# Optimization experiments

Measured on AMD Instinct MI355X. Metric: run time of the kernel, lower is better.

## Reference

```python
import jax, jax.numpy as jnp
import numpy as np

NP_, NA_, NS_ = 4096, 4096, 1
E_ = 131072
DIN, DOUT, H = 256, 64, 4
SLOPE = 0.2  # leaky relu negative slope


def _leaky(x):
    return jnp.where(x >= 0, x, SLOPE * x)


def setup_inputs() -> dict:
    key = jax.random.key(0)
    ks = iter(jax.random.split(key, 64))
    inp = {}
    inp['feat_P'] = jax.random.normal(next(ks), (NP_, DIN), jnp.float32)
    inp['feat_A'] = jax.random.normal(next(ks), (NA_, DIN), jnp.float32)
    inp['feat_state'] = jax.random.normal(next(ks), (NS_, DIN), jnp.float32)
    for name in ['P', 'A', 'p2p', 'p2a', 'a2p', 'a2a', 'p2s', 'a2s', 'in']:
        inp['W_' + name] = jax.random.normal(next(ks), (DOUT * H, DIN), jnp.float32) / np.sqrt(DIN)
        inp['b_' + name] = jax.random.normal(next(ks), (DOUT * H,), jnp.float32) * 0.01
    for name in ['p2p', 'p2a', 'a2p', 'a2a', 'p2s', 'a2s']:
        inp['att_%s_src' % name] = jax.random.normal(next(ks), (1, H, DOUT), jnp.float32) * 0.1
        inp['att_%s_dst' % name] = jax.random.normal(next(ks), (1, H, DOUT), jnp.float32) * 0.1
    for name, ns, nd in [('p2p', NP_, NP_), ('p2a', NP_, NA_), ('a2p', NA_, NP_), ('a2a', NA_, NA_)]:
        inp['e_%s_src' % name] = jax.random.randint(next(ks), (E_,), 0, ns, jnp.int32)
        inp['e_%s_dst' % name] = jax.random.randint(next(ks), (E_,), 0, nd, jnp.int32)
    inp['e_p2s_src'] = jnp.arange(NP_, dtype=jnp.int32)
    inp['e_p2s_dst'] = jnp.zeros((NP_,), jnp.int32)
    inp['e_a2s_src'] = jnp.arange(NA_, dtype=jnp.int32)
    inp['e_a2s_dst'] = jnp.zeros((NA_,), jnp.int32)
    return inp


def _msg_agg(feat_src, W, b, att_s, att_d, Wh_dst, src, dst, n_dst):
    # per-edge lossy_u_mul_e with comm_loss == 0 (noise branch dead):
    # gather src features, per-edge linear, per-edge softmax over HEADS (torch Softmax(dim=1)).
    h = feat_src[src]                                    # [E, DIN]
    Wh = (h @ W.T + b).reshape(-1, H, DOUT)              # [E, H, D]
    a_s = jnp.sum(Wh * att_s, axis=-1, keepdims=True)    # [E, H, 1]
    a_d = jnp.sum(Wh_dst[dst] * att_d, axis=-1, keepdims=True)
    attn = jax.nn.softmax(_leaky(a_s + a_d), axis=1)     # softmax over heads, as in original
    return jax.ops.segment_sum(Wh * attn, dst, num_segments=n_dst)


def _edge_softmax_agg(Wh_src, att_s, Wh_state, att_d, src, dst, n_dst):
    # dgl edge_softmax: destination-grouped stable softmax over incoming edges.
    a_s = jnp.sum(Wh_src * att_s, axis=-1, keepdims=True)[src]    # [E, H, 1]
    a_d = jnp.sum(Wh_state * att_d, axis=-1, keepdims=True)[dst]  # [E, H, 1]
    e = _leaky(a_s + a_d)
    m = jax.ops.segment_max(e, dst, num_segments=n_dst)
    ex = jnp.exp(e - m[dst])
    den = jax.ops.segment_sum(ex, dst, num_segments=n_dst)
    a = ex / den[dst]
    return jax.ops.segment_sum(Wh_src[src] * a, dst, num_segments=n_dst)


def reference(feat_P, feat_A, feat_state,
              W_P, b_P, W_A, b_A, W_p2p, b_p2p, W_p2a, b_p2a, W_a2p, b_a2p,
              W_a2a, b_a2a, W_p2s, b_p2s, W_a2s, b_a2s, W_in, b_in,
              att_p2p_src, att_p2p_dst, att_p2a_src, att_p2a_dst,
              att_a2p_src, att_a2p_dst, att_a2a_src, att_a2a_dst,
              att_p2s_src, att_p2s_dst, att_a2s_src, att_a2s_dst,
              e_p2p_src, e_p2p_dst, e_p2a_src, e_p2a_dst,
              e_a2p_src, e_a2p_dst, e_a2a_src, e_a2a_dst,
              e_p2s_src, e_p2s_dst, e_a2s_src, e_a2s_dst):
    Whp = (feat_P @ W_P.T + b_P).reshape(NP_, H, DOUT)
    Wha = (feat_A @ W_A.T + b_A).reshape(NA_, H, DOUT)
    Whp2s = (feat_P @ W_p2s.T + b_p2s).reshape(NP_, H, DOUT)
    Wha2s = (feat_A @ W_a2s.T + b_a2s).reshape(NA_, H, DOUT)
    Whin = (feat_state @ W_in.T + b_in).reshape(NS_, H, DOUT)

    ft_p2p = _msg_agg(feat_P, W_p2p, b_p2p, att_p2p_src, att_p2p_dst, Whp, e_p2p_src, e_p2p_dst, NP_)
    ft_p2a = _msg_agg(feat_P, W_p2a, b_p2a, att_p2a_src, att_p2a_dst, Wha, e_p2a_src, e_p2a_dst, NA_)
    ft_a2p = _msg_agg(feat_A, W_a2p, b_a2p, att_a2p_src, att_a2p_dst, Whp, e_a2p_src, e_a2p_dst, NP_)
    ft_a2a = _msg_agg(feat_A, W_a2a, b_a2a, att_a2a_src, att_a2a_dst, Wha, e_a2a_src, e_a2a_dst, NA_)

    ft_p2s = _edge_softmax_agg(Whp2s, att_p2s_src, Whin, att_p2s_dst, e_p2s_src, e_p2s_dst, NS_)
    ft_a2s = _edge_softmax_agg(Wha2s, att_a2s_src, Whin, att_a2s_dst, e_a2s_src, e_a2s_dst, NS_)

    h_P = jax.nn.relu(Whp + ft_p2p + ft_a2p)
    h_A = jax.nn.relu(Wha + ft_p2a + ft_a2a)
    h_S = jax.nn.relu(Whin + ft_p2s + ft_a2s)
    return (h_P, h_A, h_S)
```

## Files before the change

kernel.cpp:

```cpp
#include <hip/hip_runtime.h>

#define NPA   4096
#define DHD   256
#define EDG   131072
#define OS    4104
#define TBL_SZ ((size_t)NPA * DHD)

#define B_AH    ((size_t)0)
#define B_WH    (B_AH + 2 * TBL_SZ * 2)
#define B_TBL   (B_WH + (size_t)8 * 65536 * 2)
#define B_SCORE (B_TBL + 8 * TBL_SZ * 2)
#define B_CNT   (B_SCORE + (size_t)10 * NPA * 4 * 4)
#define B_OFFS  (B_CNT + (size_t)4 * NPA * 4)
#define B_CUR   (B_OFFS + (size_t)4 * OS * 4)
#define B_PKT   (B_CUR + (size_t)4 * NPA * 4)
#define B_WHIN  (B_PKT + (size_t)4 * EDG * 16)
#define B_SCD   (B_WHIN + 256 * 4)
#define B_DEN   (B_SCD + 8 * 4)
#define B_NUM   (B_DEN + 8 * 4)

typedef _Float16 half8 __attribute__((ext_vector_type(8)));
typedef _Float16 half4 __attribute__((ext_vector_type(4)));
typedef _Float16 half2v __attribute__((ext_vector_type(2)));
typedef float floatx4 __attribute__((ext_vector_type(4)));

struct CastArgs { const float* src[10]; };
struct GemmArgs {
    const float* b[8];
    const float* att0[8]; const float* att1[8];
    int sj0[8]; int sj1[8];
};
struct EdgeArgs { const int* src[4]; const int* dst[4]; };

__device__ __forceinline__ float lrelu(float x) { return x >= 0.0f ? x : 0.2f * x; }

__device__ __forceinline__ int pack2(float a, float b) {
    half2v h = {(_Float16)a, (_Float16)b};
    return __builtin_bit_cast(int, h);
}
__device__ __forceinline__ half2v bc2(int v) { return __builtin_bit_cast(half2v, v); }

__device__ __forceinline__ half2v asplat(const int4& p, int head) {
    int w = (head & 2) ? p.z : p.y;
    int b = (head & 1) ? ((w >> 16) & 0xffff) : (w & 0xffff);
    return bc2(b | (b << 16));
}

__global__ __launch_bounds__(256) void cast_kernel(CastArgs ca, _Float16* __restrict__ dst) {
    size_t i4 = ((size_t)blockIdx.x * 256 + threadIdx.x) * 4;
    const float* s; size_t off;
    if (i4 < TBL_SZ)            { s = ca.src[0]; off = i4; }
    else if (i4 < 2 * TBL_SZ)   { s = ca.src[1]; off = i4 - TBL_SZ; }
    else { size_t r = i4 - 2 * TBL_SZ; s = ca.src[2 + (r >> 16)]; off = r & 65535; }
    float4 v = *(const float4*)(s + off);
    half4 h = {(_Float16)v.x, (_Float16)v.y, (_Float16)v.z, (_Float16)v.w};
    *(half4*)(dst + i4) = h;
}

__global__ __launch_bounds__(256) void aux_kernel(EdgeArgs ea,
        const float* __restrict__ fs, const float* __restrict__ Win,
        const float* __restrict__ bin, const float* __restrict__ attP,
        const float* __restrict__ attA,
        int* __restrict__ cnt, float* __restrict__ whin, float* __restrict__ scd) {
    int bid = blockIdx.x;
    int wave = threadIdx.x >> 6, lane = threadIdx.x & 63;
    if (bid < 64) {
        int o = bid * 4 + wave;
        float4 w = *(const float4*)&Win[(size_t)o * 256 + lane * 4];
        float4 f = *(const float4*)&fs[lane * 4];
        float v = w.x * f.x + w.y * f.y + w.z * f.z + w.w * f.w;
        for (int d = 32; d; d >>= 1) v += __shfl_xor(v, d);
        if (lane == 0) {
            v += bin[o];
            whin[o] = v;
            atomicAdd(&scd[o >> 6], v * attP[o]);
            atomicAdd(&scd[4 + (o >> 6)], v * attA[o]);
        }
        return;
    }
    int tid = (bid - 64) * 256 + threadIdx.x;
    for (int idx = tid; idx < 4 * EDG; idx += 192 * 256) {
        int r = idx >> 17;
        int e = idx & (EDG - 1);
        atomicAdd(&cnt[r * NPA + ea.dst[r][e]], 1);
    }
}

__global__ __launch_bounds__(256) void gemm_kernel(const _Float16* __restrict__ Ah,
        const _Float16* __restrict__ Whb, GemmArgs ga,
        _Float16* __restrict__ tblBase, float* __restrict__ score) {
    int j = blockIdx.x >> 6;
    int mt = blockIdx.x & 63;
    int w = threadIdx.x >> 6, lane = threadIdx.x & 63;
    int quad = lane >> 4, l16 = lane & 15;
    const _Float16* A = Ah + (size_t)(j >> 2) * TBL_SZ;
    const _Float16* W = Whb + (size_t)j * 65536;
    const float* bias = ga.b[j];
    _Float16* out = tblBase + (size_t)j * TBL_SZ;
    int mr0 = mt * 64;
    int nc0 = w * 64;
    const _Float16* ap[4];
    const _Float16* bp[4];
#pragma unroll
    for (int g = 0; g < 4; ++g) {
        ap[g] = A + (size_t)(mr0 + g * 16 + l16) * 256 + quad * 8;
        bp[g] = W + (size_t)(nc0 + g * 16 + l16) * 256 + quad * 8;
    }
    floatx4 acc[4][4];
#pragma unroll
    for (int rg = 0; rg < 4; ++rg)
#pragma unroll
        for (int cg = 0; cg < 4; ++cg) acc[rg][cg] = (floatx4){0, 0, 0, 0};
#pragma unroll
    for (int k0 = 0; k0 < 256; k0 += 32) {
        half8 av[4], bv[4];
#pragma unroll
        for (int g = 0; g < 4; ++g) av[g] = *(const half8*)(ap[g] + k0);
#pragma unroll
        for (int g = 0; g < 4; ++g) bv[g] = *(const half8*)(bp[g] + k0);
#pragma unroll
        for (int rg = 0; rg < 4; ++rg)
#pragma unroll
            for (int cg = 0; cg < 4; ++cg)
                acc[rg][cg] = __builtin_amdgcn_mfma_f32_16x16x32_f16(av[rg], bv[cg], acc[rg][cg], 0, 0, 0);
    }
    float bc[4];
#pragma unroll
    for (int cg = 0; cg < 4; ++cg) bc[cg] = bias[nc0 + cg * 16 + l16];
#pragma unroll
    for (int rg = 0; rg < 4; ++rg)
#pragma unroll
        for (int i = 0; i < 4; ++i) {
            int row = mr0 + rg * 16 + quad * 4 + i;
#pragma unroll
            for (int cg = 0; cg < 4; ++cg)
                out[(size_t)row * 256 + nc0 + cg * 16 + l16] = (_Float16)(acc[rg][cg][i] + bc[cg]);
        }
#pragma unroll
    for (int tt = 0; tt < 2; ++tt) {
        const float* att = tt ? ga.att1[j] : ga.att0[j];
        int sj = tt ? ga.sj1[j] : ga.sj0[j];
        if (!att) continue;
        float at[4];
#pragma unroll
        for (int cg = 0; cg < 4; ++cg) at[cg] = att[nc0 + cg * 16 + l16];
        float* sb = score + (size_t)sj * NPA * 4;
#pragma unroll
        for (int rg = 0; rg < 4; ++rg)
#pragma unroll
            for (int i = 0; i < 4; ++i) {
                float p = (acc[rg][0][i] + bc[0]) * at[0] + (acc[rg][1][i] + bc[1]) * at[1]
                        + (acc[rg][2][i] + bc[2]) * at[2] + (acc[rg][3][i] + bc[3]) * at[3];
                p += __shfl_xor(p, 1); p += __shfl_xor(p, 2);
                p += __shfl_xor(p, 4); p += __shfl_xor(p, 8);
                if (l16 == 0) {
                    int row = mr0 + rg * 16 + quad * 4 + i;
                    sb[(size_t)row * 4 + w] = p;
                }
            }
    }
}

__global__ __launch_bounds__(1024) void scan_kernel(const int* __restrict__ counts,
                                                    int* __restrict__ offs, int* __restrict__ cur) {
    int r = blockIdx.x;
    int t = threadIdx.x;
    int wave = t >> 6, lane = t & 63;
    int4 v = *(const int4*)&counts[(size_t)r * NPA + t * 4];
    int lsum = v.x + v.y + v.z + v.w;
    int s = lsum;
#pragma unroll
    for (int d = 1; d < 64; d <<= 1) {
        int u = __shfl_up(s, d);
        if (lane >= d) s += u;
    }
    __shared__ int wsum[16];
    if (lane == 63) wsum[wave] = s;
    __syncthreads();
    if (wave == 0 && lane < 16) {
        int wv = wsum[lane];
#pragma unroll
        for (int d = 1; d < 16; d <<= 1) {
            int u = __shfl_up(wv, d);
            if (lane >= d) wv += u;
        }
        wsum[lane] = wv;
    }
    __syncthreads();
    int base = (wave ? wsum[wave - 1] : 0) + s - lsum;
    int4 ov = {base, base + v.x, base + v.x + v.y, base + v.x + v.y + v.z};
    *(int4*)&offs[(size_t)r * OS + t * 4] = ov;
    *(int4*)&cur[(size_t)r * NPA + t * 4] = ov;
    if (t == 1023) offs[(size_t)r * OS + NPA] = base + lsum;
}

__global__ __launch_bounds__(256) void scatter_attn(EdgeArgs ea, const float* __restrict__ scoreBase,
        int* __restrict__ cur, int4* __restrict__ pkt) {
    int idx = (blockIdx.x * 256 + threadIdx.x) * 2;
    int r = idx >> 17;
    int e = idx & (EDG - 1);
    int2 s2 = *(const int2*)&ea.src[r][e];
    int2 d2 = *(const int2*)&ea.dst[r][e];
    const float* as = scoreBase + (size_t)r * NPA * 4;
    const float* ad = scoreBase + (size_t)(4 + r) * NPA * 4;
    float4 av0 = *(const float4*)&as[(size_t)s2.x * 4];
    float4 dv0 = *(const float4*)&ad[(size_t)d2.x * 4];
    float4 av1 = *(const float4*)&as[(size_t)s2.y * 4];
    float4 dv1 = *(const float4*)&ad[(size_t)d2.y * 4];
#pragma unroll
    for (int u = 0; u < 2; ++u) {
        float4 av = u ? av1 : av0;
        float4 dv = u ? dv1 : dv0;
        int s = u ? s2.y : s2.x;
        int d = u ? d2.y : d2.x;
        float x0 = lrelu(av.x + dv.x), x1 = lrelu(av.y + dv.y);
        float x2 = lrelu(av.z + dv.z), x3 = lrelu(av.w + dv.w);
        float m = fmaxf(fmaxf(x0, x1), fmaxf(x2, x3));
        float e0 = __expf(x0 - m), e1 = __expf(x1 - m), e2 = __expf(x2 - m), e3 = __expf(x3 - m);
        float inv = 1.0f / (e0 + e1 + e2 + e3);
        int pos = atomicAdd(&cur[r * NPA + d], 1);
        int4 pk = {s, pack2(e0 * inv, e1 * inv), pack2(e2 * inv, e3 * inv), 0};
        pkt[(size_t)r * EDG + pos] = pk;
    }
}

__global__ __launch_bounds__(256) void agg_kernel(const int* __restrict__ offs,
        const int4* __restrict__ pkt, const _Float16* __restrict__ tblBase,
        float* __restrict__ outBase) {
    int side = blockIdx.y;
    int wave = threadIdx.x >> 6, lane = threadIdx.x & 63;
    int dn = blockIdx.x * 4 + wave;
    int h = lane >> 5, l32 = lane & 31;
    int head = l32 >> 3;
    half2v accA[4] = {{0,0},{0,0},{0,0},{0,0}};
    half2v accB[4] = {{0,0},{0,0},{0,0},{0,0}};
    const int srcIdx[4] = {1, 2, 5, 6};
    const int4 z = {0, 0, 0, 0};
#pragma unroll
    for (int q = 0; q < 2; ++q) {
        int r = side + q * 2;
        const int* of = offs + (size_t)r * OS;
        const int4* pkb = pkt + (size_t)r * EDG;
        const _Float16* wh = tblBase + (size_t)srcIdx[r] * TBL_SZ;
        int beg = of[dn], end = of[dn + 1];
        int i = beg;
        int4 p0 = (i + h     < end) ? pkb[i + h]     : z;
        int4 p1 = (i + 2 + h < end) ? pkb[i + 2 + h] : z;
        int4 p2 = (i + 4 + h < end) ? pkb[i + 4 + h] : z;
        int4 p3 = (i + 6 + h < end) ? pkb[i + 6 + h] : z;
        while (i < end) {
            int ni = i + 8;
            half8 w0 = *(const half8*)(wh + (size_t)p0.x * 256 + l32 * 8);
            half8 w1 = *(const half8*)(wh + (size_t)p1.x * 256 + l32 * 8);
            half8 w2 = *(const half8*)(wh + (size_t)p2.x * 256 + l32 * 8);
            half8 w3 = *(const half8*)(wh + (size_t)p3.x * 256 + l32 * 8);
            int4 n0 = (ni + h     < end) ? pkb[ni + h]     : z;
            int4 n1 = (ni + 2 + h < end) ? pkb[ni + 2 + h] : z;
            int4 n2 = (ni + 4 + h < end) ? pkb[ni + 4 + h] : z;
            int4 n3 = (ni + 6 + h < end) ? pkb[ni + 6 + h] : z;
            half2v a0 = asplat(p0, head), a1 = asplat(p1, head);
            half2v a2 = asplat(p2, head), a3 = asplat(p3, head);
            int4 i0 = __builtin_bit_cast(int4, w0);
            int4 i1 = __builtin_bit_cast(int4, w1);
            int4 i2 = __builtin_bit_cast(int4, w2);
            int4 i3 = __builtin_bit_cast(int4, w3);
            accA[0] += bc2(i0.x) * a0; accA[1] += bc2(i0.y) * a0;
            accA[2] += bc2(i0.z) * a0; accA[3] += bc2(i0.w) * a0;
            accB[0] += bc2(i1.x) * a1; accB[1] += bc2(i1.y) * a1;
            accB[2] += bc2(i1.z) * a1; accB[3] += bc2(i1.w) * a1;
            accA[0] += bc2(i2.x) * a2; accA[1] += bc2(i2.y) * a2;
            accA[2] += bc2(i2.z) * a2; accA[3] += bc2(i2.w) * a2;
            accB[0] += bc2(i3.x) * a3; accB[1] += bc2(i3.y) * a3;
            accB[2] += bc2(i3.z) * a3; accB[3] += bc2(i3.w) * a3;
            p0 = n0; p1 = n1; p2 = n2; p3 = n3;
            i = ni;
        }
    }
    float f[8];
#pragma unroll
    for (int k = 0; k < 4; ++k) {
        half2v s = accA[k] + accB[k];
        f[2 * k] = (float)s[0];
        f[2 * k + 1] = (float)s[1];
    }
#pragma unroll
    for (int k = 0; k < 8; ++k) f[k] += __shfl_xor(f[k], 32);
    if (h == 0) {
        const _Float16* skip = tblBase + (size_t)(side * 4) * TBL_SZ + (size_t)dn * 256 + l32 * 8;
        half8 sv = *(const half8*)skip;
        float* op = outBase + ((size_t)side * NPA + dn) * 256 + l32 * 8;
        float4 o0 = {fmaxf(f[0] + (float)sv[0], 0.f), fmaxf(f[1] + (float)sv[1], 0.f),
                     fmaxf(f[2] + (float)sv[2], 0.f), fmaxf(f[3] + (float)sv[3], 0.f)};
        float4 o1 = {fmaxf(f[4] + (float)sv[4], 0.f), fmaxf(f[5] + (float)sv[5], 0.f),
                     fmaxf(f[6] + (float)sv[6], 0.f), fmaxf(f[7] + (float)sv[7], 0.f)};
        *(float4*)op = o0;
        *(float4*)(op + 4) = o1;
    }
}

__global__ __launch_bounds__(256) void state_kernel(const _Float16* __restrict__ tblBase,
        const float* __restrict__ scoreBase, const float* __restrict__ scd,
        float* __restrict__ den, float* __restrict__ num) {
    int r = blockIdx.y;
    int blk = blockIdx.x;
    int t = threadIdx.x;
    int h = t >> 6;
    const _Float16* wh = tblBase + (size_t)(r == 0 ? 3 : 7) * TBL_SZ;
    const float* as = scoreBase + (size_t)(8 + r) * NPA * 4;
    float dh = scd[r * 4 + h];
    float dsum = 0.0f, acc = 0.0f;
    for (int i = blk; i < NPA; i += 128) {
        float x = lrelu(as[(size_t)i * 4 + h] + dh);
        float w = __expf(x);
        dsum += w;
        acc += w * (float)wh[(size_t)i * 256 + t];
    }
    atomicAdd(&num[r * 256 + t], acc);
    if ((t & 63) == 0) atomicAdd(&den[r * 4 + h], dsum);
}

__global__ __launch_bounds__(256) void state_final(const float* __restrict__ whin,
        const float* __restrict__ den, const float* __restrict__ num, float* __restrict__ out) {
    int t = threadIdx.x;
    int h = t >> 6;
    float v = whin[t] + num[t] / den[h] + num[256 + t] / den[4 + h];
    out[t] = v > 0.0f ? v : 0.0f;
}

extern "C" void kernel_launch(void* const* d_in, const int* in_sizes, int n_in,
                              void* d_out, int out_size, void* d_ws, size_t ws_size,
                              hipStream_t stream) {
    auto F = [&](int i) { return (const float*)d_in[i]; };
    char* ws = (char*)d_ws;
    _Float16* Ah  = (_Float16*)(ws + B_AH);
    _Float16* Whb = (_Float16*)(ws + B_WH);
    _Float16* tbl = (_Float16*)(ws + B_TBL);
    float* score  = (float*)(ws + B_SCORE);
    int* cnt      = (int*)(ws + B_CNT);
    int* offs     = (int*)(ws + B_OFFS);
    int* cur      = (int*)(ws + B_CUR);
    int4* pkt     = (int4*)(ws + B_PKT);
    float* whin   = (float*)(ws + B_WHIN);
    float* scd    = (float*)(ws + B_SCD);
    float* den    = (float*)(ws + B_DEN);
    float* num    = (float*)(ws + B_NUM);

    (void)hipMemsetAsync(cnt, 0, (size_t)4 * NPA * 4, stream);
    (void)hipMemsetAsync(scd, 0, (8 + 8 + 512) * sizeof(float), stream);

    CastArgs ca = {{F(0), F(1), F(3), F(7), F(9), F(15), F(5), F(11), F(13), F(17)}};
    cast_kernel<<<2560, 256, 0, stream>>>(ca, Ah);

    GemmArgs ga;
    const int bIdx[8] = {4, 8, 10, 16, 6, 12, 14, 18};
    for (int j = 0; j < 8; ++j) ga.b[j] = F(bIdx[j]);
    const int a0Idx[8]  = {22, 21, 23, 29, 24, 25, 27, 31};
    const int sj0Arr[8] = { 4,  0,  1,  8,  5,  2,  3,  9};
    for (int j = 0; j < 8; ++j) {
        ga.att0[j] = F(a0Idx[j]); ga.sj0[j] = sj0Arr[j];
        ga.att1[j] = nullptr;     ga.sj1[j] = -1;
    }
    ga.att1[0] = F(26); ga.sj1[0] = 6;
    ga.att1[4] = F(28); ga.sj1[4] = 7;

    EdgeArgs ea = {{(const int*)d_in[33], (const int*)d_in[35], (const int*)d_in[37], (const int*)d_in[39]},
                   {(const int*)d_in[34], (const int*)d_in[36], (const int*)d_in[38], (const int*)d_in[40]}};

    aux_kernel<<<256, 256, 0, stream>>>(ea, F(2), F(19), F(20), F(30), F(32), cnt, whin, scd);
    gemm_kernel<<<512, 256, 0, stream>>>(Ah, Whb, ga, tbl, score);

    scan_kernel<<<4, 1024, 0, stream>>>(cnt, offs, cur);
    scatter_attn<<<1024, 256, 0, stream>>>(ea, score, cur, pkt);
    agg_kernel<<<dim3(1024, 2), 256, 0, stream>>>(offs, pkt, tbl, (float*)d_out);
    state_kernel<<<dim3(128, 2), 256, 0, stream>>>(tbl, score, scd, den, num);
    state_final<<<1, 256, 0, stream>>>(whin, den, num, (float*)d_out + 2 * TBL_SZ);
}
```

Baseline: 278.4 us.

## Move edge attention into aggregation, fuse cast/aux kernels and state finalize

The scatter pass now writes only a 4-byte source-index permutation instead of 16-byte packets carrying precomputed attention. The aggregation kernel gathers source scores itself and computes the per-head softmax there, and the destination scores are loaded once per node. The cast and aux kernels become one launch, state_final is folded into state_kernel through a last-block ticket, and the two memsets become one. This cuts launches and scatter write traffic, but adds redundant exp work and extra score gathers inside the aggregation loop. Softmax also drops max-subtraction, which could overflow on large scores.

Result: slower. 309.0 us (+11.0%).

```diff
diff --git a/kernel.cpp b/kernel.cpp
--- a/kernel.cpp
+++ b/kernel.cpp
@@ -11,13 +11,15 @@
 #define B_TBL   (B_WH + (size_t)8 * 65536 * 2)
 #define B_SCORE (B_TBL + 8 * TBL_SZ * 2)
 #define B_CNT   (B_SCORE + (size_t)10 * NPA * 4 * 4)
-#define B_OFFS  (B_CNT + (size_t)4 * NPA * 4)
-#define B_CUR   (B_OFFS + (size_t)4 * OS * 4)
-#define B_PKT   (B_CUR + (size_t)4 * NPA * 4)
-#define B_WHIN  (B_PKT + (size_t)4 * EDG * 16)
-#define B_SCD   (B_WHIN + 256 * 4)
+#define B_SCD   (B_CNT + (size_t)4 * NPA * 4)
 #define B_DEN   (B_SCD + 8 * 4)
 #define B_NUM   (B_DEN + 8 * 4)
+#define B_TKT   (B_NUM + 512 * 4)
+#define B_ZEND  (B_TKT + 16)
+#define B_OFFS  (B_ZEND)
+#define B_CUR   (B_OFFS + (size_t)4 * OS * 4)
+#define B_PERM  (B_CUR + (size_t)4 * NPA * 4)
+#define B_WHIN  (B_PERM + (size_t)4 * EDG * 4)
 
 typedef _Float16 half8 __attribute__((ext_vector_type(8)));
 typedef _Float16 half4 __attribute__((ext_vector_type(4)));
@@ -33,39 +35,40 @@
 struct EdgeArgs { const int* src[4]; const int* dst[4]; };
 
 __device__ __forceinline__ float lrelu(float x) { return x >= 0.0f ? x : 0.2f * x; }
-
-__device__ __forceinline__ int pack2(float a, float b) {
-    half2v h = {(_Float16)a, (_Float16)b};
-    return __builtin_bit_cast(int, h);
-}
 __device__ __forceinline__ half2v bc2(int v) { return __builtin_bit_cast(half2v, v); }
-
-__device__ __forceinline__ half2v asplat(const int4& p, int head) {
-    int w = (head & 2) ? p.z : p.y;
-    int b = (head & 1) ? ((w >> 16) & 0xffff) : (w & 0xffff);
-    return bc2(b | (b << 16));
-}
-
-__global__ __launch_bounds__(256) void cast_kernel(CastArgs ca, _Float16* __restrict__ dst) {
-    size_t i4 = ((size_t)blockIdx.x * 256 + threadIdx.x) * 4;
-    const float* s; size_t off;
-    if (i4 < TBL_SZ)            { s = ca.src[0]; off = i4; }
-    else if (i4 < 2 * TBL_SZ)   { s = ca.src[1]; off = i4 - TBL_SZ; }
-    else { size_t r = i4 - 2 * TBL_SZ; s = ca.src[2 + (r >> 16)]; off = r & 65535; }
-    float4 v = *(const float4*)(s + off);
-    half4 h = {(_Float16)v.x, (_Float16)v.y, (_Float16)v.z, (_Float16)v.w};
-    *(half4*)(dst + i4) = h;
-}
-
-__global__ __launch_bounds__(256) void aux_kernel(EdgeArgs ea,
+__device__ __forceinline__ half2v cvt2(float a, float b) {
+    return __builtin_bit_cast(half2v, __builtin_amdgcn_cvt_pkrtz(a, b));
+}
+
+__device__ __forceinline__ float attn_head(float4 g, float4 ad, int head) {
+    float e0 = __expf(lrelu(g.x + ad.x));
+    float e1 = __expf(lrelu(g.y + ad.y));
+    float e2 = __expf(lrelu(g.z + ad.z));
+    float e3 = __expf(lrelu(g.w + ad.w));
+    float sel = (head & 2) ? ((head & 1) ? e3 : e2) : ((head & 1) ? e1 : e0);
+    return sel * __builtin_amdgcn_rcpf(e0 + e1 + e2 + e3);
+}
+
+__global__ __launch_bounds__(256) void prep_kernel(CastArgs ca, EdgeArgs ea,
         const float* __restrict__ fs, const float* __restrict__ Win,
         const float* __restrict__ bin, const float* __restrict__ attP,
-        const float* __restrict__ attA,
+        const float* __restrict__ attA, _Float16* __restrict__ dst,
         int* __restrict__ cnt, float* __restrict__ whin, float* __restrict__ scd) {
     int bid = blockIdx.x;
+    if (bid < 2560) {
+        size_t i4 = ((size_t)bid * 256 + threadIdx.x) * 4;
+        const float* s; size_t off;
+        if (i4 < TBL_SZ)            { s = ca.src[0]; off = i4; }
+        else if (i4 < 2 * TBL_SZ)   { s = ca.src[1]; off = i4 - TBL_SZ; }
+        else { size_t r = i4 - 2 * TBL_SZ; s = ca.src[2 + (r >> 16)]; off = r & 65535; }
+        float4 v = *(const float4*)(s + off);
+        half4 hh = {(_Float16)v.x, (_Float16)v.y, (_Float16)v.z, (_Float16)v.w};
+        *(half4*)(dst + i4) = hh;
+        return;
+    }
     int wave = threadIdx.x >> 6, lane = threadIdx.x & 63;
-    if (bid < 64) {
-        int o = bid * 4 + wave;
+    if (bid < 2624) {
+        int o = (bid - 2560) * 4 + wave;
         float4 w = *(const float4*)&Win[(size_t)o * 256 + lane * 4];
         float4 f = *(const float4*)&fs[lane * 4];
         float v = w.x * f.x + w.y * f.y + w.z * f.z + w.w * f.w;
@@ -78,7 +81,7 @@
         }
         return;
     }
-    int tid = (bid - 64) * 256 + threadIdx.x;
+    int tid = (bid - 2624) * 256 + threadIdx.x;
     for (int idx = tid; idx < 4 * EDG; idx += 192 * 256) {
         int r = idx >> 17;
         int e = idx & (EDG - 1);
@@ -194,39 +197,22 @@
     if (t == 1023) offs[(size_t)r * OS + NPA] = base + lsum;
 }
 
-__global__ __launch_bounds__(256) void scatter_attn(EdgeArgs ea, const float* __restrict__ scoreBase,
-        int* __restrict__ cur, int4* __restrict__ pkt) {
+__global__ __launch_bounds__(256) void scatter_kernel(EdgeArgs ea, int* __restrict__ cur,
+                                                      int* __restrict__ perm) {
     int idx = (blockIdx.x * 256 + threadIdx.x) * 2;
     int r = idx >> 17;
     int e = idx & (EDG - 1);
     int2 s2 = *(const int2*)&ea.src[r][e];
     int2 d2 = *(const int2*)&ea.dst[r][e];
-    const float* as = scoreBase + (size_t)r * NPA * 4;
-    const float* ad = scoreBase + (size_t)(4 + r) * NPA * 4;
-    float4 av0 = *(const float4*)&as[(size_t)s2.x * 4];
-    float4 dv0 = *(const float4*)&ad[(size_t)d2.x * 4];
-    float4 av1 = *(const float4*)&as[(size_t)s2.y * 4];
-    float4 dv1 = *(const float4*)&ad[(size_t)d2.y * 4];
-#pragma unroll
-    for (int u = 0; u < 2; ++u) {
-        float4 av = u ? av1 : av0;
-        float4 dv = u ? dv1 : dv0;
-        int s = u ? s2.y : s2.x;
-        int d = u ? d2.y : d2.x;
-        float x0 = lrelu(av.x + dv.x), x1 = lrelu(av.y + dv.y);
-        float x2 = lrelu(av.z + dv.z), x3 = lrelu(av.w + dv.w);
-        float m = fmaxf(fmaxf(x0, x1), fmaxf(x2, x3));
-        float e0 = __expf(x0 - m), e1 = __expf(x1 - m), e2 = __expf(x2 - m), e3 = __expf(x3 - m);
-        float inv = 1.0f / (e0 + e1 + e2 + e3);
-        int pos = atomicAdd(&cur[r * NPA + d], 1);
-        int4 pk = {s, pack2(e0 * inv, e1 * inv), pack2(e2 * inv, e3 * inv), 0};
-        pkt[(size_t)r * EDG + pos] = pk;
-    }
+    int p0 = atomicAdd(&cur[r * NPA + d2.x], 1);
+    perm[(size_t)r * EDG + p0] = s2.x;
+    int p1 = atomicAdd(&cur[r * NPA + d2.y], 1);
+    perm[(size_t)r * EDG + p1] = s2.y;
 }
 
 __global__ __launch_bounds__(256) void agg_kernel(const int* __restrict__ offs,
-        const int4* __restrict__ pkt, const _Float16* __restrict__ tblBase,
-        float* __restrict__ outBase) {
+        const int* __restrict__ perm, const float* __restrict__ score,
+        const _Float16* __restrict__ tblBase, float* __restrict__ outBase) {
     int side = blockIdx.y;
     int wave = threadIdx.x >> 6, lane = threadIdx.x & 63;
     int dn = blockIdx.x * 4 + wave;
@@ -235,44 +221,53 @@
     half2v accA[4] = {{0,0},{0,0},{0,0},{0,0}};
     half2v accB[4] = {{0,0},{0,0},{0,0},{0,0}};
     const int srcIdx[4] = {1, 2, 5, 6};
-    const int4 z = {0, 0, 0, 0};
 #pragma unroll
     for (int q = 0; q < 2; ++q) {
         int r = side + q * 2;
         const int* of = offs + (size_t)r * OS;
-        const int4* pkb = pkt + (size_t)r * EDG;
+        const int* pm = perm + (size_t)r * EDG;
+        const float* ss = score + (size_t)r * NPA * 4;
+        float4 ad = *(const float4*)&score[(size_t)(4 + r) * NPA * 4 + (size_t)dn * 4];
         const _Float16* wh = tblBase + (size_t)srcIdx[r] * TBL_SZ;
         int beg = of[dn], end = of[dn + 1];
         int i = beg;
-        int4 p0 = (i + h     < end) ? pkb[i + h]     : z;
-        int4 p1 = (i + 2 + h < end) ? pkb[i + 2 + h] : z;
-        int4 p2 = (i + 4 + h < end) ? pkb[i + 4 + h] : z;
-        int4 p3 = (i + 6 + h < end) ? pkb[i + 6 + h] : z;
+        int s0 = (i + h     < end) ? pm[i + h]     : 0;
+        int s1 = (i + 2 + h < end) ? pm[i + 2 + h] : 0;
+        int s2 = (i + 4 + h < end) ? pm[i + 4 + h] : 0;
+        int s3 = (i + 6 + h < end) ? pm[i + 6 + h] : 0;
         while (i < end) {
             int ni = i + 8;
-            half8 w0 = *(const half8*)(wh + (size_t)p0.x * 256 + l32 * 8);
-            half8 w1 = *(const half8*)(wh + (size_t)p1.x * 256 + l32 * 8);
-            half8 w2 = *(const half8*)(wh + (size_t)p2.x * 256 + l32 * 8);
-            half8 w3 = *(const half8*)(wh + (size_t)p3.x * 256 + l32 * 8);
-            int4 n0 = (ni + h     < end) ? pkb[ni + h]     : z;
-            int4 n1 = (ni + 2 + h < end) ? pkb[ni + 2 + h] : z;
-            int4 n2 = (ni + 4 + h < end) ? pkb[ni + 4 + h] : z;
-            int4 n3 = (ni + 6 + h < end) ? pkb[ni + 6 + h] : z;
-            half2v a0 = asplat(p0, head), a1 = asplat(p1, head);
-            half2v a2 = asplat(p2, head), a3 = asplat(p3, head);
+            float4 g0 = *(const float4*)&ss[(size_t)s0 * 4];
+            float4 g1 = *(const float4*)&ss[(size_t)s1 * 4];
+            float4 g2 = *(const float4*)&ss[(size_t)s2 * 4];
+            float4 g3 = *(const float4*)&ss[(size_t)s3 * 4];
+            half8 w0 = *(const half8*)(wh + (size_t)s0 * 256 + l32 * 8);
+            half8 w1 = *(const half8*)(wh + (size_t)s1 * 256 + l32 * 8);
+            half8 w2 = *(const half8*)(wh + (size_t)s2 * 256 + l32 * 8);
+            half8 w3 = *(const half8*)(wh + (size_t)s3 * 256 + l32 * 8);
+            int t0 = (ni + h     < end) ? pm[ni + h]     : 0;
+            int t1 = (ni + 2 + h < end) ? pm[ni + 2 + h] : 0;
+            int t2 = (ni + 4 + h < end) ? pm[ni + 4 + h] : 0;
+            int t3 = (ni + 6 + h < end) ? pm[ni + 6 + h] : 0;
+            float a0 = (i + h     < end) ? attn_head(g0, ad, head) : 0.f;
+            float a1 = (i + 2 + h < end) ? attn_head(g1, ad, head) : 0.f;
+            float a2 = (i + 4 + h < end) ? attn_head(g2, ad, head) : 0.f;
+            float a3 = (i + 6 + h < end) ? attn_head(g3, ad, head) : 0.f;
+            half2v ha0 = cvt2(a0, a0), ha1 = cvt2(a1, a1);
+            half2v ha2 = cvt2(a2, a2), ha3 = cvt2(a3, a3);
             int4 i0 = __builtin_bit_cast(int4, w0);
             int4 i1 = __builtin_bit_cast(int4, w1);
             int4 i2 = __builtin_bit_cast(int4, w2);
             int4 i3 = __builtin_bit_cast(int4, w3);
-            accA[0] += bc2(i0.x) * a0; accA[1] += bc2(i0.y) * a0;
-            accA[2] += bc2(i0.z) * a0; accA[3] += bc2(i0.w) * a0;
-            accB[0] += bc2(i1.x) * a1; accB[1] += bc2(i1.y) * a1;
-            accB[2] += bc2(i1.z) * a1; accB[3] += bc2(i1.w) * a1;
-            accA[0] += bc2(i2.x) * a2; accA[1] += bc2(i2.y) * a2;
-            accA[2] += bc2(i2.z) * a2; accA[3] += bc2(i2.w) * a2;
-            accB[0] += bc2(i3.x) * a3; accB[1] += bc2(i3.y) * a3;
-            accB[2] += bc2(i3.z) * a3; accB[3] += bc2(i3.w) * a3;
-            p0 = n0; p1 = n1; p2 = n2; p3 = n3;
+            accA[0] += bc2(i0.x) * ha0; accA[1] += bc2(i0.y) * ha0;
+            accA[2] += bc2(i0.z) * ha0; accA[3] += bc2(i0.w) * ha0;
+            accB[0] += bc2(i1.x) * ha1; accB[1] += bc2(i1.y) * ha1;
+            accB[2] += bc2(i1.z) * ha1; accB[3] += bc2(i1.w) * ha1;
+            accA[0] += bc2(i2.x) * ha2; accA[1] += bc2(i2.y) * ha2;
+            accA[2] += bc2(i2.z) * ha2; accA[3] += bc2(i2.w) * ha2;
+            accB[0] += bc2(i3.x) * ha3; accB[1] += bc2(i3.y) * ha3;
+            accB[2] += bc2(i3.z) * ha3; accB[3] += bc2(i3.w) * ha3;
+            s0 = t0; s1 = t1; s2 = t2; s3 = t3;
             i = ni;
         }
     }
@@ -299,14 +294,15 @@
 }
 
 __global__ __launch_bounds__(256) void state_kernel(const _Float16* __restrict__ tblBase,
-        const float* __restrict__ scoreBase, const float* __restrict__ scd,
-        float* __restrict__ den, float* __restrict__ num) {
+        const float* __restrict__ score, const float* __restrict__ scd,
+        float* __restrict__ den, float* __restrict__ num,
+        const float* __restrict__ whin, float* __restrict__ out, int* __restrict__ ticket) {
     int r = blockIdx.y;
     int blk = blockIdx.x;
     int t = threadIdx.x;
     int h = t >> 6;
     const _Float16* wh = tblBase + (size_t)(r == 0 ? 3 : 7) * TBL_SZ;
-    const float* as = scoreBase + (size_t)(8 + r) * NPA * 4;
+    const float* as = score + (size_t)(8 + r) * NPA * 4;
     float dh = scd[r * 4 + h];
     float dsum = 0.0f, acc = 0.0f;
     for (int i = blk; i < NPA; i += 128) {
@@ -317,14 +313,18 @@
     }
     atomicAdd(&num[r * 256 + t], acc);
     if ((t & 63) == 0) atomicAdd(&den[r * 4 + h], dsum);
-}
-
-__global__ __launch_bounds__(256) void state_final(const float* __restrict__ whin,
-        const float* __restrict__ den, const float* __restrict__ num, float* __restrict__ out) {
-    int t = threadIdx.x;
-    int h = t >> 6;
-    float v = whin[t] + num[t] / den[h] + num[256 + t] / den[4 + h];
-    out[t] = v > 0.0f ? v : 0.0f;
+    __threadfence();
+    __shared__ int last;
+    if (t == 0) last = (atomicAdd(ticket, 1) == 255);
+    __syncthreads();
+    if (last) {
+        float n0 = atomicAdd(&num[t], 0.f);
+        float n1 = atomicAdd(&num[256 + t], 0.f);
+        float d0 = atomicAdd(&den[h], 0.f);
+        float d1 = atomicAdd(&den[4 + h], 0.f);
+        float v = whin[t] + n0 / d0 + n1 / d1;
+        out[t] = fmaxf(v, 0.f);
+    }
 }
 
 extern "C" void kernel_launch(void* const* d_in, const int* in_sizes, int n_in,
@@ -337,19 +337,23 @@
     _Float16* tbl = (_Float16*)(ws + B_TBL);
     float* score  = (float*)(ws + B_SCORE);
     int* cnt      = (int*)(ws + B_CNT);
-    int* offs     = (int*)(ws + B_OFFS);
-    int* cur      = (int*)(ws + B_CUR);
-    int4* pkt     = (int4*)(ws + B_PKT);
-    float* whin   = (float*)(ws + B_WHIN);
     float* scd    = (float*)(ws + B_SCD);
     float* den    = (float*)(ws + B_DEN);
     float* num    = (float*)(ws + B_NUM);
-
-    (void)hipMemsetAsync(cnt, 0, (size_t)4 * NPA * 4, stream);
-    (void)hipMemsetAsync(scd, 0, (8 + 8 + 512) * sizeof(float), stream);
+    int* ticket   = (int*)(ws + B_TKT);
+    int* offs     = (int*)(ws + B_OFFS);
+    int* cur      = (int*)(ws + B_CUR);
+    int* perm     = (int*)(ws + B_PERM);
+    float* whin   = (float*)(ws + B_WHIN);
+
+    (void)hipMemsetAsync(ws + B_CNT, 0, B_ZEND - B_CNT, stream);
 
     CastArgs ca = {{F(0), F(1), F(3), F(7), F(9), F(15), F(5), F(11), F(13), F(17)}};
-    cast_kernel<<<2560, 256, 0, stream>>>(ca, Ah);
+    EdgeArgs ea = {{(const int*)d_in[33], (const int*)d_in[35], (const int*)d_in[37], (const int*)d_in[39]},
+                   {(const int*)d_in[34], (const int*)d_in[36], (const int*)d_in[38], (const int*)d_in[40]}};
+
+    prep_kernel<<<2816, 256, 0, stream>>>(ca, ea, F(2), F(19), F(20), F(30), F(32),
+                                          Ah, cnt, whin, scd);
 
     GemmArgs ga;
     const int bIdx[8] = {4, 8, 10, 16, 6, 12, 14, 18};
@@ -363,15 +367,10 @@
     ga.att1[0] = F(26); ga.sj1[0] = 6;
     ga.att1[4] = F(28); ga.sj1[4] = 7;
 
-    EdgeArgs ea = {{(const int*)d_in[33], (const int*)d_in[35], (const int*)d_in[37], (const int*)d_in[39]},
-                   {(const int*)d_in[34], (const int*)d_in[36], (const int*)d_in[38], (const int*)d_in[40]}};
-
-    aux_kernel<<<256, 256, 0, stream>>>(ea, F(2), F(19), F(20), F(30), F(32), cnt, whin, scd);
     gemm_kernel<<<512, 256, 0, stream>>>(Ah, Whb, ga, tbl, score);
-
     scan_kernel<<<4, 1024, 0, stream>>>(cnt, offs, cur);
-    scatter_attn<<<1024, 256, 0, stream>>>(ea, score, cur, pkt);
-    agg_kernel<<<dim3(1024, 2), 256, 0, stream>>>(offs, pkt, tbl, (float*)d_out);
-    state_kernel<<<dim3(128, 2), 256, 0, stream>>>(tbl, score, scd, den, num);
-    state_final<<<1, 256, 0, stream>>>(whin, den, num, (float*)d_out + 2 * TBL_SZ);
-}
+    scatter_kernel<<<1024, 256, 0, stream>>>(ea, cur, perm);
+    agg_kernel<<<dim3(1024, 2), 256, 0, stream>>>(offs, perm, score, tbl, (float*)d_out);
+    state_kernel<<<dim3(128, 2), 256, 0, stream>>>(tbl, score, scd, den, num, whin,
+                                                   (float*)d_out + 2 * TBL_SZ, ticket);
+}
```

## Fuse cast and aux kernels, use LDS histogram, merge memsets

Applied to the files above, without the earlier changes.

Merges the fp16 cast kernel and the aux kernel (state projection plus in-degree counting) into one prep kernel. This removes one launch, and the two memsets become a single memset by making the zeroed buffers contiguous. Degree counting now builds a per-block shared-memory histogram over 16K-edge chunks and flushes nonzero bins with global atomics. This replaces per-edge global atomics and cuts atomic contention, at the cost of 16KB of LDS per block and only 32 blocks doing the counting.

Measured after the change: 269.6 us. -3.1%, faster.

```diff
diff --git a/kernel.cpp b/kernel.cpp
--- a/kernel.cpp
+++ b/kernel.cpp
@@ -11,13 +11,14 @@
 #define B_TBL   (B_WH + (size_t)8 * 65536 * 2)
 #define B_SCORE (B_TBL + 8 * TBL_SZ * 2)
 #define B_CNT   (B_SCORE + (size_t)10 * NPA * 4 * 4)
-#define B_OFFS  (B_CNT + (size_t)4 * NPA * 4)
+#define B_SCD   (B_CNT + (size_t)4 * NPA * 4)
+#define B_DEN   (B_SCD + 8 * 4)
+#define B_NUM   (B_DEN + 8 * 4)
+#define B_ZEND  (B_NUM + 512 * 4)
+#define B_OFFS  (B_ZEND)
 #define B_CUR   (B_OFFS + (size_t)4 * OS * 4)
 #define B_PKT   (B_CUR + (size_t)4 * NPA * 4)
 #define B_WHIN  (B_PKT + (size_t)4 * EDG * 16)
-#define B_SCD   (B_WHIN + 256 * 4)
-#define B_DEN   (B_SCD + 8 * 4)
-#define B_NUM   (B_DEN + 8 * 4)
 
 typedef _Float16 half8 __attribute__((ext_vector_type(8)));
 typedef _Float16 half4 __attribute__((ext_vector_type(4)));
@@ -46,26 +47,36 @@
     return bc2(b | (b << 16));
 }
 
-__global__ __launch_bounds__(256) void cast_kernel(CastArgs ca, _Float16* __restrict__ dst) {
-    size_t i4 = ((size_t)blockIdx.x * 256 + threadIdx.x) * 4;
-    const float* s; size_t off;
-    if (i4 < TBL_SZ)            { s = ca.src[0]; off = i4; }
-    else if (i4 < 2 * TBL_SZ)   { s = ca.src[1]; off = i4 - TBL_SZ; }
-    else { size_t r = i4 - 2 * TBL_SZ; s = ca.src[2 + (r >> 16)]; off = r & 65535; }
-    float4 v = *(const float4*)(s + off);
-    half4 h = {(_Float16)v.x, (_Float16)v.y, (_Float16)v.z, (_Float16)v.w};
-    *(half4*)(dst + i4) = h;
-}
-
-__global__ __launch_bounds__(256) void aux_kernel(EdgeArgs ea,
+__global__ __launch_bounds__(256) void prep_kernel(CastArgs ca, EdgeArgs ea,
         const float* __restrict__ fs, const float* __restrict__ Win,
         const float* __restrict__ bin, const float* __restrict__ attP,
-        const float* __restrict__ attA,
+        const float* __restrict__ attA, _Float16* __restrict__ dst,
         int* __restrict__ cnt, float* __restrict__ whin, float* __restrict__ scd) {
+    __shared__ int hist[NPA];
     int bid = blockIdx.x;
-    int wave = threadIdx.x >> 6, lane = threadIdx.x & 63;
-    if (bid < 64) {
-        int o = bid * 4 + wave;
+    int tid = threadIdx.x;
+    if (bid < 32) {
+        int r = bid >> 3;
+        int chunk = bid & 7;
+        const int* dp = ea.dst[r] + chunk * 16384;
+#pragma unroll
+        for (int i = 0; i < 16; ++i) hist[tid + i * 256] = 0;
+        __syncthreads();
+#pragma unroll
+        for (int k = 0; k < 64; ++k)
+            atomicAdd(&hist[dp[k * 256 + tid]], 1);
+        __syncthreads();
+        int* cr = cnt + r * NPA;
+#pragma unroll
+        for (int i = 0; i < 16; ++i) {
+            int v = hist[tid + i * 256];
+            if (v) atomicAdd(&cr[tid + i * 256], v);
+        }
+        return;
+    }
+    int wave = tid >> 6, lane = tid & 63;
+    if (bid < 96) {
+        int o = (bid - 32) * 4 + wave;
         float4 w = *(const float4*)&Win[(size_t)o * 256 + lane * 4];
         float4 f = *(const float4*)&fs[lane * 4];
         float v = w.x * f.x + w.y * f.y + w.z * f.z + w.w * f.w;
@@ -78,12 +89,14 @@
         }
         return;
     }
-    int tid = (bid - 64) * 256 + threadIdx.x;
-    for (int idx = tid; idx < 4 * EDG; idx += 192 * 256) {
-        int r = idx >> 17;
-        int e = idx & (EDG - 1);
-        atomicAdd(&cnt[r * NPA + ea.dst[r][e]], 1);
-    }
+    size_t i4 = ((size_t)(bid - 96) * 256 + tid) * 4;
+    const float* s; size_t off;
+    if (i4 < TBL_SZ)            { s = ca.src[0]; off = i4; }
+    else if (i4 < 2 * TBL_SZ)   { s = ca.src[1]; off = i4 - TBL_SZ; }
+    else { size_t r = i4 - 2 * TBL_SZ; s = ca.src[2 + (r >> 16)]; off = r & 65535; }
+    float4 v = *(const float4*)(s + off);
+    half4 hh = {(_Float16)v.x, (_Float16)v.y, (_Float16)v.z, (_Float16)v.w};
+    *(half4*)(dst + i4) = hh;
 }
 
 __global__ __launch_bounds__(256) void gemm_kernel(const _Float16* __restrict__ Ah,
@@ -337,19 +350,22 @@
     _Float16* tbl = (_Float16*)(ws + B_TBL);
     float* score  = (float*)(ws + B_SCORE);
     int* cnt      = (int*)(ws + B_CNT);
+    float* scd    = (float*)(ws + B_SCD);
+    float* den    = (float*)(ws + B_DEN);
+    float* num    = (float*)(ws + B_NUM);
     int* offs     = (int*)(ws + B_OFFS);
     int* cur      = (int*)(ws + B_CUR);
     int4* pkt     = (int4*)(ws + B_PKT);
     float* whin   = (float*)(ws + B_WHIN);
-    float* scd    = (float*)(ws + B_SCD);
-    float* den    = (float*)(ws + B_DEN);
-    float* num    = (float*)(ws + B_NUM);
-
-    (void)hipMemsetAsync(cnt, 0, (size_t)4 * NPA * 4, stream);
-    (void)hipMemsetAsync(scd, 0, (8 + 8 + 512) * sizeof(float), stream);
+
+    (void)hipMemsetAsync(ws + B_CNT, 0, B_ZEND - B_CNT, stream);
 
     CastArgs ca = {{F(0), F(1), F(3), F(7), F(9), F(15), F(5), F(11), F(13), F(17)}};
-    cast_kernel<<<2560, 256, 0, stream>>>(ca, Ah);
+    EdgeArgs ea = {{(const int*)d_in[33], (const int*)d_in[35], (const int*)d_in[37], (const int*)d_in[39]},
+                   {(const int*)d_in[34], (const int*)d_in[36], (const int*)d_in[38], (const int*)d_in[40]}};
+
+    prep_kernel<<<2656, 256, 0, stream>>>(ca, ea, F(2), F(19), F(20), F(30), F(32),
+                                          Ah, cnt, whin, scd);
 
     GemmArgs ga;
     const int bIdx[8] = {4, 8, 10, 16, 6, 12, 14, 18};
@@ -363,12 +379,7 @@
     ga.att1[0] = F(26); ga.sj1[0] = 6;
     ga.att1[4] = F(28); ga.sj1[4] = 7;
 
-    EdgeArgs ea = {{(const int*)d_in[33], (const int*)d_in[35], (const int*)d_in[37], (const int*)d_in[39]},
-                   {(const int*)d_in[34], (const int*)d_in[36], (const int*)d_in[38], (const int*)d_in[40]}};
-
-    aux_kernel<<<256, 256, 0, stream>>>(ea, F(2), F(19), F(20), F(30), F(32), cnt, whin, scd);
     gemm_kernel<<<512, 256, 0, stream>>>(Ah, Whb, ga, tbl, score);
-
     scan_kernel<<<4, 1024, 0, stream>>>(cnt, offs, cur);
     scatter_attn<<<1024, 256, 0, stream>>>(ea, score, cur, pkt);
     agg_kernel<<<dim3(1024, 2), 256, 0, stream>>>(offs, pkt, tbl, (float*)d_out);
```
